# Optimization experiments

Measured on AMD Instinct MI355X. Metric: run time of the kernel, lower is better.

The kernel has to match this reference:

```python
import jax, jax.numpy as jnp
import numpy as np
import math

RES = 320
DECIMATION = 4
M = RES * RES // DECIMATION  # 25600 trajectory points
OVERSAMP = 1.25
WIDTH = 4
BETA = math.pi * (((WIDTH / OVERSAMP) * (OVERSAMP - 0.5)) ** 2 - 0.8) ** 0.5
B = 16


def setup_inputs() -> dict:
    key = jax.random.key(0)
    k1, k2 = jax.random.split(key)
    k_space_input = jax.random.normal(k1, (B, 1, RES, RES, 2), dtype=jnp.float32)
    # learnable k-space trajectory, coords in [-RES/2, RES/2)
    trajectory = (jax.random.uniform(k2, (M, 2), dtype=jnp.float32) - 0.5) * RES
    return {"k_space_input": k_space_input, "trajectory": trajectory}


def _grid_sample_bilinear(img, traj):
    # img: [B, C, H, W]; traj: [M, 2] = (x, y) in [-res/2, res/2]
    # Matches torch grid_sample(align_corners=True, padding_mode='zeros')
    # after normalizing traj by (res/2).
    Bn, C, H, W = img.shape
    gx = traj[:, 0] / (W / 2)
    gy = traj[:, 1] / (H / 2)
    px = (gx + 1.0) * 0.5 * (W - 1)
    py = (gy + 1.0) * 0.5 * (H - 1)
    x0 = jnp.floor(px)
    y0 = jnp.floor(py)
    wx1 = px - x0
    wy1 = py - y0
    out = jnp.zeros((Bn, C, traj.shape[0]), img.dtype)
    for dy in (0, 1):
        for dx in (0, 1):
            xi = x0 + dx
            yi = y0 + dy
            w = (wx1 if dx else 1.0 - wx1) * (wy1 if dy else 1.0 - wy1)
            inb = (xi >= 0) & (xi < W) & (yi >= 0) & (yi < H)
            xc = jnp.clip(xi, 0, W - 1).astype(jnp.int32)
            yc = jnp.clip(yi, 0, H - 1).astype(jnp.int32)
            out = out + img[:, :, yc, xc] * (w * inb)[None, None, :]
    return out  # [B, C, M]


def _kb_weight(delta, half):
    # Kaiser-Bessel interpolation kernel (sigpy convention, 1/width factor per dim)
    x = delta / half
    t = jnp.maximum(1.0 - x * x, 0.0)
    return jnp.i0(BETA * jnp.sqrt(t)) / WIDTH


def _nufft_adjoint(y, coord, H, W):
    # y: [B, M] complex64; coord: [M,2], coord[:,0]->H axis, coord[:,1]->W axis
    osH = math.ceil(OVERSAMP * H)
    osW = math.ceil(OVERSAMP * W)
    scale = jnp.array([osH / H, osW / W], jnp.float32)
    shift = jnp.array([osH // 2, osW // 2], jnp.float32)
    c = coord * scale + shift  # scaled to oversampled-grid coords
    half = WIDTH / 2.0
    start = jnp.ceil(c - half)                       # [M,2]
    offs = jnp.arange(WIDTH, dtype=jnp.float32)
    idx = start[:, :, None] + offs                   # [M,2,WIDTH]
    w = _kb_weight(c[:, :, None] - idx, half)        # [M,2,WIDTH]
    iy = idx[:, 0].astype(jnp.int32) % osH           # [M,WIDTH]
    ix = idx[:, 1].astype(jnp.int32) % osW
    ww = w[:, 0, :, None] * w[:, 1, None, :]         # [M,WIDTH,WIDTH]
    flat = (iy[:, :, None] * osW + ix[:, None, :]).reshape(-1)  # [M*WIDTH^2]
    Bn = y.shape[0]
    contrib = (y[:, :, None, None] * ww[None]).reshape(Bn, -1)  # [B, M*WIDTH^2]
    grid = jnp.zeros((Bn, osH * osW), y.dtype).at[:, flat].add(contrib)
    grid = grid.reshape(Bn, osH, osW)
    # centered unnormalized-to-ortho IFFT (sigpy scaling)
    img = jnp.fft.fftshift(
        jnp.fft.ifft2(jnp.fft.ifftshift(grid, axes=(-2, -1)), axes=(-2, -1)),
        axes=(-2, -1))
    img = img * ((osH * osW) / math.sqrt(H * W))
    sy = osH // 2 - H // 2
    sx = osW // 2 - W // 2
    img = img[:, sy:sy + H, sx:sx + W]  # center crop

    def apod(n, os_n):
        a = jnp.sqrt(jnp.maximum(
            BETA ** 2 - (np.pi * WIDTH * (jnp.arange(n, dtype=jnp.float32) - n // 2) / os_n) ** 2,
            1e-12))
        return a / jnp.sinh(a)

    img = img * apod(H, osH)[:, None] * apod(W, osW)[None, :]
    return img  # [B, H, W] complex


def reference(k_space_input, trajectory):
    # [B,1,H,W,2] -> [B,2,H,W] (real/imag channels)
    ksp = jnp.transpose(k_space_input, (0, 1, 4, 2, 3))[:, 0]
    sub = _grid_sample_bilinear(ksp, trajectory)          # [B,2,M]
    y = (sub[:, 0] + 1j * sub[:, 1]).astype(jnp.complex64)
    img = _nufft_adjoint(y, trajectory, ksp.shape[-2], ksp.shape[-1])
    out = jnp.stack([img.real, img.imag], axis=1)          # [B,2,H,W]
    return out[:, None]                                    # [B,1,2,H,W]
```

## Files before the change

### kernel.cpp

```cpp
#include <hip/hip_runtime.h>

#define NPTS   25600
#define NB     16
#define NRES   320
#define OS     400
#define NCELL  (OS * OS)
#define CAP    16
#define MAXOVF 4096

#define NJ     8
#define FFTTH  512
#define LSTRV  404

#define BETA_F (3.14159265358979f * 2.22710574513201f)

__device__ __forceinline__ float bessel_i0f(float x) {
    float ax = fabsf(x);
    if (ax < 3.75f) {
        float t = (ax * ax) * (1.0f / 14.0625f);
        return 1.0f + t * (3.5156229f + t * (3.0899424f + t * (1.2067492f +
                     t * (0.2659732f + t * (0.0360768f + t * 0.0045813f)))));
    } else {
        float t = 3.75f / ax;
        return (expf(ax) * rsqrtf(ax)) *
               (0.39894228f + t * (0.01328592f + t * (0.00225319f + t * (-0.00157565f +
                t * (0.00916281f + t * (-0.02057706f + t * (0.02635537f +
                t * (-0.01647633f + t * 0.00392377f))))))));
    }
}

struct OvfEntry { int cell; int m; float w; float pad; };

__global__ __launch_bounds__(256)
void k_sample(const float* __restrict__ ksp,
              const float* __restrict__ traj,
              float2* __restrict__ val)
{
    int gid = blockIdx.x * blockDim.x + threadIdx.x;
    if (gid >= NPTS * NB) return;
    int b = gid & 15;
    int m = gid >> 4;

    float tx = traj[2 * m + 0];
    float ty = traj[2 * m + 1];

    float px = (tx * (1.0f / 160.0f) + 1.0f) * 0.5f * 319.0f;
    float py = (ty * (1.0f / 160.0f) + 1.0f) * 0.5f * 319.0f;
    float fx0 = floorf(px), fy0 = floorf(py);
    int x0 = (int)fx0, y0 = (int)fy0;
    float wx1 = px - fx0, wy1 = py - fy0;
    float wx0 = 1.0f - wx1, wy0 = 1.0f - wy1;
    x0 = min(max(x0, 0), NRES - 1);
    y0 = min(max(y0, 0), NRES - 1);
    int x1 = min(x0 + 1, NRES - 1);
    int y1 = min(y0 + 1, NRES - 1);

    const float2* base = (const float2*)ksp + (size_t)b * NRES * NRES;
    float2 v00 = base[y0 * NRES + x0];
    float2 v01 = base[y0 * NRES + x1];
    float2 v10 = base[y1 * NRES + x0];
    float2 v11 = base[y1 * NRES + x1];
    float sr = (v00.x * wx0 + v01.x * wx1) * wy0 + (v10.x * wx0 + v11.x * wx1) * wy1;
    float si = (v00.y * wx0 + v01.y * wx1) * wy0 + (v10.y * wx0 + v11.y * wx1) * wy1;

    val[gid] = make_float2(sr, si);
}

__global__ __launch_bounds__(256)
void k_taps(const float* __restrict__ traj,
            int* __restrict__ cursor,
            float2* __restrict__ entries,
            int* __restrict__ ovf_cnt,
            OvfEntry* __restrict__ ovf)
{
    int m = blockIdx.x * blockDim.x + threadIdx.x;
    if (m >= NPTS) return;

    float tx = traj[2 * m + 0];
    float ty = traj[2 * m + 1];
    float c0 = tx * 1.25f + 200.0f;
    float c1 = ty * 1.25f + 200.0f;
    float s0 = ceilf(c0 - 2.0f);
    float s1 = ceilf(c1 - 2.0f);

    float w0[4], w1[4];
    int   i0[4], i1[4];
#pragma unroll
    for (int t = 0; t < 4; t++) {
        float id0 = s0 + (float)t;
        float d0 = (c0 - id0) * 0.5f;
        float t0 = fmaxf(1.0f - d0 * d0, 0.0f);
        w0[t] = bessel_i0f(BETA_F * sqrtf(t0)) * 0.25f;
        i0[t] = (((int)id0) + OS) % OS;

        float id1 = s1 + (float)t;
        float d1 = (c1 - id1) * 0.5f;
        float t1 = fmaxf(1.0f - d1 * d1, 0.0f);
        w1[t] = bessel_i0f(BETA_F * sqrtf(t1)) * 0.25f;
        i1[t] = (((int)id1) + OS) % OS;
    }

#pragma unroll
    for (int t0 = 0; t0 < 4; t0++) {
#pragma unroll
        for (int t1 = 0; t1 < 4; t1++) {
            int cell = i1[t1] * OS + i0[t0];
            float w = w0[t0] * w1[t1];
            int slot = atomicAdd(&cursor[cell], 1);
            if (slot < CAP) {
                entries[slot * NCELL + cell] = make_float2(__int_as_float(m), w);
            } else {
                int oi = atomicAdd(ovf_cnt, 1);
                if (oi < MAXOVF) { ovf[oi].cell = cell; ovf[oi].m = m; ovf[oi].w = w; }
            }
        }
    }
}

__global__ __launch_bounds__(256)
void k_gather(const int* __restrict__ cursor,
              const float2* __restrict__ entries,
              const float4* __restrict__ val4,
              float2* __restrict__ grid,
              const int* __restrict__ ovf_cnt,
              const OvfEntry* __restrict__ ovf)
{
    int cell = blockIdx.x * blockDim.x + threadIdx.x;
    if (cell >= NCELL) return;
    int cnt_raw = cursor[cell];
    int cnt = min(cnt_raw, CAP);

    float4 acc[8];
#pragma unroll
    for (int q = 0; q < 8; q++) acc[q] = make_float4(0.f, 0.f, 0.f, 0.f);

    for (int k = 0; k < cnt; k++) {
        float2 e = entries[k * NCELL + cell];
        int m = __float_as_int(e.x);
        float w = e.y;
        const float4* v = val4 + (size_t)m * 8;
#pragma unroll
        for (int q = 0; q < 8; q++) {
            float4 x = v[q];
            acc[q].x = fmaf(w, x.x, acc[q].x);
            acc[q].y = fmaf(w, x.y, acc[q].y);
            acc[q].z = fmaf(w, x.z, acc[q].z);
            acc[q].w = fmaf(w, x.w, acc[q].w);
        }
    }

    if (cnt_raw > CAP) {
        int n = min(*ovf_cnt, MAXOVF);
        for (int i = 0; i < n; i++) {
            if (ovf[i].cell != cell) continue;
            int m = ovf[i].m;
            float w = ovf[i].w;
            const float4* v = val4 + (size_t)m * 8;
#pragma unroll
            for (int q = 0; q < 8; q++) {
                float4 x = v[q];
                acc[q].x = fmaf(w, x.x, acc[q].x);
                acc[q].y = fmaf(w, x.y, acc[q].y);
                acc[q].z = fmaf(w, x.z, acc[q].z);
                acc[q].w = fmaf(w, x.w, acc[q].w);
            }
        }
    }

#pragma unroll
    for (int q = 0; q < 8; q++) {
        grid[(size_t)(2 * q + 0) * NCELL + cell] = make_float2(acc[q].x, acc[q].y);
        grid[(size_t)(2 * q + 1) * NCELL + cell] = make_float2(acc[q].z, acc[q].w);
    }
}


__device__ __forceinline__ float apodf(int i) {
    float t = (float)(i - 160) * 0.031415926535897932f;
    float a = sqrtf(fmaxf(BETA_F * BETA_F - t * t, 1e-12f));
    return a / sinhf(a);
}

__global__ __launch_bounds__(FFTTH)
void k_fft_pass_a(const float* __restrict__ grid, float* __restrict__ At)
{
    __shared__ float2 A[NJ * LSTRV];
    __shared__ float4 B4[NJ * 200];
    __shared__ float2 E20t[20];
    __shared__ float2 E400p[424];
    int tid = threadIdx.x;
    int b = blockIdx.y;
    int j0 = blockIdx.x * NJ;

    for (int t = tid; t < 400; t += FFTTH) {
        float sn, cs;
        sincosf((float)t * 0.015707963267948966f, &sn, &cs);
        E400p[t + (t >> 4)] = make_float2(cs, sn);
    }
    if (tid < 20) {
        float sn, cs;
        sincosf((float)tid * 0.3141592653589793f, &sn, &cs);
        E20t[tid] = make_float2(cs, sn);
    }
    const float2* g = (const float2*)grid + ((size_t)b * OS + j0) * OS;
    for (int o = tid; o < NJ * OS; o += FFTTH) {
        int r = o / OS, i = o - r * OS;
        A[r * LSTRV + i] = g[r * OS + i];
    }
    __syncthreads();

    for (int o = tid; o < NJ * 200; o += FFTTH) {
        int r = o / 200, rem = o - r * 200;
        int j = rem / 20, n2 = rem - j * 20;
        const float2* Al = &A[r * LSTRV];
        float4 outv;
        if (j == 0) {
            float2 a0 = Al[n2], a1 = Al[n2 + 200];
            outv = make_float4(a0.x, a0.y, a1.x, a1.y);
        } else {
            float2 a0 = Al[n2 + 20 * j], a1 = Al[n2 + 20 * (20 - j)];
            outv = make_float4(a0.x + a1.x, a0.y + a1.y, a0.x - a1.x, a0.y - a1.y);
        }
        B4[r * 200 + j * 20 + n2] = outv;
    }
    __syncthreads();

    for (int o = tid; o < NJ * 200; o += FFTTH) {
        int r = o / 200, rem = o - r * 200;
        int k1h = rem / 20, n2 = rem - k1h * 20;
        const float4* Bl = &B4[r * 200];
        float4 b0 = Bl[n2];
        float2* Ar_ = &A[r * LSTRV + 20 * n2];
        if (k1h == 0) {
            float b_r = b0.x + b0.z, b_i = b0.y + b0.w;
            float a0r = 0.f, a0i = 0.f, d0r = 0.f, d0i = 0.f;
#pragma unroll
            for (int j = 1; j <= 9; j++) {
                float4 P = Bl[j * 20 + n2];
                a0r += P.x; a0i += P.y;
                float sg = (j & 1) ? -1.f : 1.f;
                d0r = fmaf(sg, P.x, d0r); d0i = fmaf(sg, P.y, d0i);
            }
            Ar_[0] = make_float2(b_r + a0r, b_i + a0i);
            int ti = 10 * n2;
            float2 tw = E400p[ti + (ti >> 4)];
            float xr = b_r + d0r, xi = b_i + d0i;
            Ar_[10] = make_float2(xr * tw.x - xi * tw.y, xr * tw.y + xi * tw.x);
        } else {
            float sgn = (k1h & 1) ? -1.f : 1.f;
            float b_r = fmaf(sgn, b0.z, b0.x), b_i = fmaf(sgn, b0.w, b0.y);
            float2 ek = E20t[k1h];
            float c = ek.x, s = ek.y;
            float Asr = 0.f, Asi = 0.f, Bsr = 0.f, Bsi = 0.f;
#pragma unroll
            for (int j = 1; j <= 9; j++) {
                float4 P = Bl[j * 20 + n2];
                Asr = fmaf(c, P.x, Asr); Asi = fmaf(c, P.y, Asi);
                Bsr = fmaf(s, P.w, Bsr); Bsi = fmaf(s, P.z, Bsi);
                float cn = c * ek.x - s * ek.y;
                s = c * ek.y + s * ek.x;
                c = cn;
            }
            float x1r = b_r + Asr - Bsr, x1i = b_i + Asi + Bsi;
            float x2r = b_r + Asr + Bsr, x2i = b_i + Asi - Bsi;
            int t1 = n2 * k1h;
            int t2 = n2 * (20 - k1h);
            float2 tw1 = E400p[t1 + (t1 >> 4)];
            float2 tw2 = E400p[t2 + (t2 >> 4)];
            Ar_[k1h]      = make_float2(x1r * tw1.x - x1i * tw1.y, x1r * tw1.y + x1i * tw1.x);
            Ar_[20 - k1h] = make_float2(x2r * tw2.x - x2i * tw2.y, x2r * tw2.y + x2i * tw2.x);
        }
    }
    __syncthreads();

    for (int o = tid; o < NJ * 200; o += FFTTH) {
        int r = o / 200, rem = o - r * 200;
        int j = rem / 20, k1 = rem - j * 20;
        const float2* Sl = &A[r * LSTRV];
        float4 outv;
        if (j == 0) {
            float2 a0 = Sl[k1], a1 = Sl[200 + k1];
            outv = make_float4(a0.x, a0.y, a1.x, a1.y);
        } else {
            float2 a0 = Sl[20 * j + k1], a1 = Sl[20 * (20 - j) + k1];
            outv = make_float4(a0.x + a1.x, a0.y + a1.y, a0.x - a1.x, a0.y - a1.y);
        }
        B4[r * 200 + j * 20 + k1] = outv;
    }
    __syncthreads();

    for (int o = tid; o < NJ * 180; o += FFTTH) {
        int r = o / 180, rem = o - r * 180;
        int k2h = rem / 20, k1 = rem - k2h * 20;
        const float4* Bl = &B4[r * 200];
        float4 b0 = Bl[k1];
        float2* Ar_ = &A[r * LSTRV];
        if (k2h == 0) {
            float b_r = b0.x + b0.z, b_i = b0.y + b0.w;
            float a0r = 0.f, a0i = 0.f;
#pragma unroll
            for (int j = 1; j <= 9; j++) {
                float4 P = Bl[j * 20 + k1];
                a0r += P.x; a0i += P.y;
            }
            Ar_[k1] = make_float2(b_r + a0r, b_i + a0i);
        } else {
            float sgn = (k2h & 1) ? -1.f : 1.f;
            float b_r = fmaf(sgn, b0.z, b0.x), b_i = fmaf(sgn, b0.w, b0.y);
            float2 ek = E20t[k2h];
            float c = ek.x, s = ek.y;
            float Asr = 0.f, Asi = 0.f, Bsr = 0.f, Bsi = 0.f;
#pragma unroll
            for (int j = 1; j <= 9; j++) {
                float4 P = Bl[j * 20 + k1];
                Asr = fmaf(c, P.x, Asr); Asi = fmaf(c, P.y, Asi);
                Bsr = fmaf(s, P.w, Bsr); Bsi = fmaf(s, P.z, Bsi);
                float cn = c * ek.x - s * ek.y;
                s = c * ek.y + s * ek.x;
                c = cn;
            }
            if (k2h <= 7)
                Ar_[20 * k2h + k1] = make_float2(b_r + Asr - Bsr, b_i + Asi + Bsi);
            Ar_[320 - 20 * k2h + k1] = make_float2(b_r + Asr + Bsr, b_i + Asi - Bsi);
        }
    }
    __syncthreads();

    float2* At2 = (float2*)At;
    for (int o = tid; o < 320 * NJ; o += FFTTH) {
        int uc = o >> 3, r = o & 7;
        At2[((size_t)b * 320 + uc) * OS + j0 + r] = A[r * LSTRV + uc];
    }
}

__global__ __launch_bounds__(FFTTH)
void k_fft_pass_b(const float* __restrict__ At, float* __restrict__ out)
{
    __shared__ float2 A[NJ * LSTRV];
    __shared__ float4 B4[NJ * 200];
    __shared__ float2 E20t[20];
    __shared__ float2 E400p[424];
    __shared__ float apodT[320];
    int tid = threadIdx.x;
    int b = blockIdx.y;
    int uc0 = blockIdx.x * NJ;

    for (int t = tid; t < 400; t += FFTTH) {
        float sn, cs;
        sincosf((float)t * 0.015707963267948966f, &sn, &cs);
        E400p[t + (t >> 4)] = make_float2(cs, sn);
    }
    if (tid < 20) {
        float sn, cs;
        sincosf((float)tid * 0.3141592653589793f, &sn, &cs);
        E20t[tid] = make_float2(cs, sn);
    }
    for (int t = tid; t < 320; t += FFTTH) apodT[t] = apodf(t);

    const float2* a = (const float2*)At + ((size_t)b * 320 + uc0) * OS;
    for (int o = tid; o < NJ * OS; o += FFTTH) {
        int r = o / OS, j = o - r * OS;
        A[r * LSTRV + j] = a[r * OS + j];
    }
    __syncthreads();

    for (int o = tid; o < NJ * 200; o += FFTTH) {
        int r = o / 200, rem = o - r * 200;
        int j = rem / 20, n2 = rem - j * 20;
        const float2* Al = &A[r * LSTRV];
        float4 outv;
        if (j == 0) {
            float2 a0 = Al[n2], a1 = Al[n2 + 200];
            outv = make_float4(a0.x, a0.y, a1.x, a1.y);
        } else {
            float2 a0 = Al[n2 + 20 * j], a1 = Al[n2 + 20 * (20 - j)];
            outv = make_float4(a0.x + a1.x, a0.y + a1.y, a0.x - a1.x, a0.y - a1.y);
        }
        B4[r * 200 + j * 20 + n2] = outv;
    }
    __syncthreads();

    for (int o = tid; o < NJ * 200; o += FFTTH) {
        int r = o / 200, rem = o - r * 200;
        int k1h = rem / 20, n2 = rem - k1h * 20;
        const float4* Bl = &B4[r * 200];
        float4 b0 = Bl[n2];
        float2* Ar_ = &A[r * LSTRV + 20 * n2];
        if (k1h == 0) {
            float b_r = b0.x + b0.z, b_i = b0.y + b0.w;
            float a0r = 0.f, a0i = 0.f, d0r = 0.f, d0i = 0.f;
#pragma unroll
            for (int j = 1; j <= 9; j++) {
                float4 P = Bl[j * 20 + n2];
                a0r += P.x; a0i += P.y;
                float sg = (j & 1) ? -1.f : 1.f;
                d0r = fmaf(sg, P.x, d0r); d0i = fmaf(sg, P.y, d0i);
            }
            Ar_[0] = make_float2(b_r + a0r, b_i + a0i);
            int ti = 10 * n2;
            float2 tw = E400p[ti + (ti >> 4)];
            float xr = b_r + d0r, xi = b_i + d0i;
            Ar_[10] = make_float2(xr * tw.x - xi * tw.y, xr * tw.y + xi * tw.x);
        } else {
            float sgn = (k1h & 1) ? -1.f : 1.f;
            float b_r = fmaf(sgn, b0.z, b0.x), b_i = fmaf(sgn, b0.w, b0.y);
            float2 ek = E20t[k1h];
            float c = ek.x, s = ek.y;
            float Asr = 0.f, Asi = 0.f, Bsr = 0.f, Bsi = 0.f;
#pragma unroll
            for (int j = 1; j <= 9; j++) {
                float4 P = Bl[j * 20 + n2];
                Asr = fmaf(c, P.x, Asr); Asi = fmaf(c, P.y, Asi);
                Bsr = fmaf(s, P.w, Bsr); Bsi = fmaf(s, P.z, Bsi);
                float cn = c * ek.x - s * ek.y;
                s = c * ek.y + s * ek.x;
                c = cn;
            }
            float x1r = b_r + Asr - Bsr, x1i = b_i + Asi + Bsi;
            float x2r = b_r + Asr + Bsr, x2i = b_i + Asi - Bsi;
            int t1 = n2 * k1h;
            int t2 = n2 * (20 - k1h);
            float2 tw1 = E400p[t1 + (t1 >> 4)];
            float2 tw2 = E400p[t2 + (t2 >> 4)];
            Ar_[k1h]      = make_float2(x1r * tw1.x - x1i * tw1.y, x1r * tw1.y + x1i * tw1.x);
            Ar_[20 - k1h] = make_float2(x2r * tw2.x - x2i * tw2.y, x2r * tw2.y + x2i * tw2.x);
        }
    }
    __syncthreads();

    for (int o = tid; o < NJ * 200; o += FFTTH) {
        int r = o / 200, rem = o - r * 200;
        int j = rem / 20, k1 = rem - j * 20;
        const float2* Sl = &A[r * LSTRV];
        float4 outv;
        if (j == 0) {
            float2 a0 = Sl[k1], a1 = Sl[200 + k1];
            outv = make_float4(a0.x, a0.y, a1.x, a1.y);
        } else {
            float2 a0 = Sl[20 * j + k1], a1 = Sl[20 * (20 - j) + k1];
            outv = make_float4(a0.x + a1.x, a0.y + a1.y, a0.x - a1.x, a0.y - a1.y);
        }
        B4[r * 200 + j * 20 + k1] = outv;
    }
    __syncthreads();

    for (int o = tid; o < NJ * 180; o += FFTTH) {
        int r = o / 180, rem = o - r * 180;
        int k2h = rem / 20, k1 = rem - k2h * 20;
        const float4* Bl = &B4[r * 200];
        float4 b0 = Bl[k1];
        int y = uc0 + r + 160; if (y >= 320) y -= 320;
        float apy = (1.0f / 320.0f) * apodT[y];
        float* o0 = out + (((size_t)b * 2 + 0) * NRES + y) * NRES;
        float* o1 = out + (((size_t)b * 2 + 1) * NRES + y) * NRES;
        if (k2h == 0) {
            float b_r = b0.x + b0.z, b_i = b0.y + b0.w;
            float a0r = 0.f, a0i = 0.f;
#pragma unroll
            for (int j = 1; j <= 9; j++) {
                float4 P = Bl[j * 20 + k1];
                a0r += P.x; a0i += P.y;
            }
            int vc = k1;
            int x = vc + 160; if (x >= 320) x -= 320;
            float sg = ((x + y) & 1) ? -1.0f : 1.0f;
            float sc = sg * apy * apodT[x];
            o0[x] = (b_r + a0r) * sc;
            o1[x] = (b_i + a0i) * sc;
        } else {
            float sgn = (k2h & 1) ? -1.f : 1.f;
            float b_r = fmaf(sgn, b0.z, b0.x), b_i = fmaf(sgn, b0.w, b0.y);
            float2 ek = E20t[k2h];
            float c = ek.x, s = ek.y;
            float Asr = 0.f, Asi = 0.f, Bsr = 0.f, Bsi = 0.f;
#pragma unroll
            for (int j = 1; j <= 9; j++) {
                float4 P = Bl[j * 20 + k1];
                Asr = fmaf(c, P.x, Asr); Asi = fmaf(c, P.y, Asi);
                Bsr = fmaf(s, P.w, Bsr); Bsi = fmaf(s, P.z, Bsi);
                float cn = c * ek.x - s * ek.y;
                s = c * ek.y + s * ek.x;
                c = cn;
            }
            if (k2h <= 7) {
                int vc = 20 * k2h + k1;
                int x = vc + 160; if (x >= 320) x -= 320;
                float sg = ((x + y) & 1) ? -1.0f : 1.0f;
                float sc = sg * apy * apodT[x];
                o0[x] = (b_r + Asr - Bsr) * sc;
                o1[x] = (b_i + Asi + Bsi) * sc;
            }
            {
                int vc = 320 - 20 * k2h + k1;
                int x = vc + 160; if (x >= 320) x -= 320;
                float sg = ((x + y) & 1) ? -1.0f : 1.0f;
                float sc = sg * apy * apodT[x];
                o0[x] = (b_r + Asr + Bsr) * sc;
                o1[x] = (b_i + Asi - Bsi) * sc;
            }
        }
    }
}

extern "C" void kernel_launch(void* const* d_in, const int* in_sizes, int n_in,
                              void* d_out, int out_size, void* d_ws, size_t ws_size,
                              hipStream_t stream) {
    const float* ksp  = (const float*)d_in[0];
    const float* traj = (const float*)d_in[1];
    float* out = (float*)d_out;

    float* grid = (float*)d_ws;
    float* At   = grid + (size_t)NB * NCELL * 2;
    float2* entries = (float2*)At;
    float2* val = (float2*)(At + (size_t)NB * NCELL * 2);
    int* cursor  = (int*)(val + (size_t)NPTS * NB);
    int* ovf_cnt = cursor + NCELL;
    OvfEntry* ovf = (OvfEntry*)(ovf_cnt + 16);

    hipMemsetAsync(cursor, 0, (NCELL + 16) * sizeof(int), stream);

    k_sample    <<<dim3((NPTS * NB) / 256), 256, 0, stream>>>(ksp, traj, val);
    k_taps      <<<dim3(NPTS / 256), 256, 0, stream>>>(traj, cursor, entries, ovf_cnt, ovf);
    k_gather    <<<dim3((NCELL + 255) / 256), 256, 0, stream>>>(cursor, entries, (const float4*)val,
                                                                (float2*)grid, ovf_cnt, ovf);
    k_fft_pass_a<<<dim3(OS / NJ, NB),  FFTTH, 0, stream>>>(grid, At);
    k_fft_pass_b<<<dim3(320 / NJ, NB), FFTTH, 0, stream>>>(At, out);
}
```

Before: 155.9 us.

## Merge sample and tap kernels; fuse gridding gather into first FFT pass

Combines the bilinear sampling and Kaiser-Bessel tap-binning kernels into one launch split by block index. Removes the separate gather kernel and the intermediate oversampled grid buffer by having the first FFT pass gather each cell's contributions directly into shared memory. This saves two launches and a full grid write and read. In exchange, each FFT block re-reads the cursor and entry lists once per batch (16 times in total instead of once), using scalar float2 value loads.

```diff
diff --git a/kernel.cpp b/kernel.cpp
--- a/kernel.cpp
+++ b/kernel.cpp
@@ -32,145 +32,86 @@
 struct OvfEntry { int cell; int m; float w; float pad; };
 
 __global__ __launch_bounds__(256)
-void k_sample(const float* __restrict__ ksp,
-              const float* __restrict__ traj,
-              float2* __restrict__ val)
+void k_sample_taps(const float* __restrict__ ksp,
+                   const float* __restrict__ traj,
+                   float2* __restrict__ val,
+                   int* __restrict__ cursor,
+                   float2* __restrict__ entries,
+                   int* __restrict__ ovf_cnt,
+                   OvfEntry* __restrict__ ovf)
 {
-    int gid = blockIdx.x * blockDim.x + threadIdx.x;
-    if (gid >= NPTS * NB) return;
-    int b = gid & 15;
-    int m = gid >> 4;
-
-    float tx = traj[2 * m + 0];
-    float ty = traj[2 * m + 1];
-
-    float px = (tx * (1.0f / 160.0f) + 1.0f) * 0.5f * 319.0f;
-    float py = (ty * (1.0f / 160.0f) + 1.0f) * 0.5f * 319.0f;
-    float fx0 = floorf(px), fy0 = floorf(py);
-    int x0 = (int)fx0, y0 = (int)fy0;
-    float wx1 = px - fx0, wy1 = py - fy0;
-    float wx0 = 1.0f - wx1, wy0 = 1.0f - wy1;
-    x0 = min(max(x0, 0), NRES - 1);
-    y0 = min(max(y0, 0), NRES - 1);
-    int x1 = min(x0 + 1, NRES - 1);
-    int y1 = min(y0 + 1, NRES - 1);
-
-    const float2* base = (const float2*)ksp + (size_t)b * NRES * NRES;
-    float2 v00 = base[y0 * NRES + x0];
-    float2 v01 = base[y0 * NRES + x1];
-    float2 v10 = base[y1 * NRES + x0];
-    float2 v11 = base[y1 * NRES + x1];
-    float sr = (v00.x * wx0 + v01.x * wx1) * wy0 + (v10.x * wx0 + v11.x * wx1) * wy1;
-    float si = (v00.y * wx0 + v01.y * wx1) * wy0 + (v10.y * wx0 + v11.y * wx1) * wy1;
-
-    val[gid] = make_float2(sr, si);
-}
-
-__global__ __launch_bounds__(256)
-void k_taps(const float* __restrict__ traj,
-            int* __restrict__ cursor,
-            float2* __restrict__ entries,
-            int* __restrict__ ovf_cnt,
-            OvfEntry* __restrict__ ovf)
-{
-    int m = blockIdx.x * blockDim.x + threadIdx.x;
-    if (m >= NPTS) return;
-
-    float tx = traj[2 * m + 0];
-    float ty = traj[2 * m + 1];
-    float c0 = tx * 1.25f + 200.0f;
-    float c1 = ty * 1.25f + 200.0f;
-    float s0 = ceilf(c0 - 2.0f);
-    float s1 = ceilf(c1 - 2.0f);
-
-    float w0[4], w1[4];
-    int   i0[4], i1[4];
-#pragma unroll
-    for (int t = 0; t < 4; t++) {
-        float id0 = s0 + (float)t;
-        float d0 = (c0 - id0) * 0.5f;
-        float t0 = fmaxf(1.0f - d0 * d0, 0.0f);
-        w0[t] = bessel_i0f(BETA_F * sqrtf(t0)) * 0.25f;
-        i0[t] = (((int)id0) + OS) % OS;
-
-        float id1 = s1 + (float)t;
-        float d1 = (c1 - id1) * 0.5f;
-        float t1 = fmaxf(1.0f - d1 * d1, 0.0f);
-        w1[t] = bessel_i0f(BETA_F * sqrtf(t1)) * 0.25f;
-        i1[t] = (((int)id1) + OS) % OS;
-    }
-
-#pragma unroll
-    for (int t0 = 0; t0 < 4; t0++) {
-#pragma unroll
-        for (int t1 = 0; t1 < 4; t1++) {
-            int cell = i1[t1] * OS + i0[t0];
-            float w = w0[t0] * w1[t1];
-            int slot = atomicAdd(&cursor[cell], 1);
-            if (slot < CAP) {
-                entries[slot * NCELL + cell] = make_float2(__int_as_float(m), w);
-            } else {
-                int oi = atomicAdd(ovf_cnt, 1);
-                if (oi < MAXOVF) { ovf[oi].cell = cell; ovf[oi].m = m; ovf[oi].w = w; }
-            }
-        }
-    }
-}
-
-__global__ __launch_bounds__(256)
-void k_gather(const int* __restrict__ cursor,
-              const float2* __restrict__ entries,
-              const float4* __restrict__ val4,
-              float2* __restrict__ grid,
-              const int* __restrict__ ovf_cnt,
-              const OvfEntry* __restrict__ ovf)
-{
-    int cell = blockIdx.x * blockDim.x + threadIdx.x;
-    if (cell >= NCELL) return;
-    int cnt_raw = cursor[cell];
-    int cnt = min(cnt_raw, CAP);
-
-    float4 acc[8];
-#pragma unroll
-    for (int q = 0; q < 8; q++) acc[q] = make_float4(0.f, 0.f, 0.f, 0.f);
-
-    for (int k = 0; k < cnt; k++) {
-        float2 e = entries[k * NCELL + cell];
-        int m = __float_as_int(e.x);
-        float w = e.y;
-        const float4* v = val4 + (size_t)m * 8;
-#pragma unroll
-        for (int q = 0; q < 8; q++) {
-            float4 x = v[q];
-            acc[q].x = fmaf(w, x.x, acc[q].x);
-            acc[q].y = fmaf(w, x.y, acc[q].y);
-            acc[q].z = fmaf(w, x.z, acc[q].z);
-            acc[q].w = fmaf(w, x.w, acc[q].w);
-        }
-    }
-
-    if (cnt_raw > CAP) {
-        int n = min(*ovf_cnt, MAXOVF);
-        for (int i = 0; i < n; i++) {
-            if (ovf[i].cell != cell) continue;
-            int m = ovf[i].m;
-            float w = ovf[i].w;
-            const float4* v = val4 + (size_t)m * 8;
-#pragma unroll
-            for (int q = 0; q < 8; q++) {
-                float4 x = v[q];
-                acc[q].x = fmaf(w, x.x, acc[q].x);
-                acc[q].y = fmaf(w, x.y, acc[q].y);
-                acc[q].z = fmaf(w, x.z, acc[q].z);
-                acc[q].w = fmaf(w, x.w, acc[q].w);
-            }
-        }
-    }
-
-#pragma unroll
-    for (int q = 0; q < 8; q++) {
-        grid[(size_t)(2 * q + 0) * NCELL + cell] = make_float2(acc[q].x, acc[q].y);
-        grid[(size_t)(2 * q + 1) * NCELL + cell] = make_float2(acc[q].z, acc[q].w);
+    int blk = blockIdx.x;
+    if (blk < 1600) {
+        int gid = blk * 256 + threadIdx.x;
+        int b = gid & 15;
+        int m = gid >> 4;
+
+        float tx = traj[2 * m + 0];
+        float ty = traj[2 * m + 1];
+
+        float px = (tx * (1.0f / 160.0f) + 1.0f) * 0.5f * 319.0f;
+        float py = (ty * (1.0f / 160.0f) + 1.0f) * 0.5f * 319.0f;
+        float fx0 = floorf(px), fy0 = floorf(py);
+        int x0 = (int)fx0, y0 = (int)fy0;
+        float wx1 = px - fx0, wy1 = py - fy0;
+        float wx0 = 1.0f - wx1, wy0 = 1.0f - wy1;
+        x0 = min(max(x0, 0), NRES - 1);
+        y0 = min(max(y0, 0), NRES - 1);
+        int x1 = min(x0 + 1, NRES - 1);
+        int y1 = min(y0 + 1, NRES - 1);
+
+        const float2* base = (const float2*)ksp + (size_t)b * NRES * NRES;
+        float2 v00 = base[y0 * NRES + x0];
+        float2 v01 = base[y0 * NRES + x1];
+        float2 v10 = base[y1 * NRES + x0];
+        float2 v11 = base[y1 * NRES + x1];
+        float sr = (v00.x * wx0 + v01.x * wx1) * wy0 + (v10.x * wx0 + v11.x * wx1) * wy1;
+        float si = (v00.y * wx0 + v01.y * wx1) * wy0 + (v10.y * wx0 + v11.y * wx1) * wy1;
+
+        val[gid] = make_float2(sr, si);
+    } else {
+        int m = (blk - 1600) * 256 + threadIdx.x;
+        if (m >= NPTS) return;
+
+        float tx = traj[2 * m + 0];
+        float ty = traj[2 * m + 1];
+        float c0 = tx * 1.25f + 200.0f;
+        float c1 = ty * 1.25f + 200.0f;
+        float s0 = ceilf(c0 - 2.0f);
+        float s1 = ceilf(c1 - 2.0f);
+
+        float w0[4], w1[4];
+        int   i0[4], i1[4];
+#pragma unroll
+        for (int t = 0; t < 4; t++) {
+            float id0 = s0 + (float)t;
+            float d0 = (c0 - id0) * 0.5f;
+            float t0 = fmaxf(1.0f - d0 * d0, 0.0f);
+            w0[t] = bessel_i0f(BETA_F * sqrtf(t0)) * 0.25f;
+            i0[t] = (((int)id0) + OS) % OS;
+
+            float id1 = s1 + (float)t;
+            float d1 = (c1 - id1) * 0.5f;
+            float t1 = fmaxf(1.0f - d1 * d1, 0.0f);
+            w1[t] = bessel_i0f(BETA_F * sqrtf(t1)) * 0.25f;
+            i1[t] = (((int)id1) + OS) % OS;
+        }
+
+#pragma unroll
+        for (int t0 = 0; t0 < 4; t0++) {
+#pragma unroll
+            for (int t1 = 0; t1 < 4; t1++) {
+                int cell = i1[t1] * OS + i0[t0];
+                float w = w0[t0] * w1[t1];
+                int slot = atomicAdd(&cursor[cell], 1);
+                if (slot < CAP) {
+                    entries[(size_t)slot * NCELL + cell] = make_float2(__int_as_float(m), w);
+                } else {
+                    int oi = atomicAdd(ovf_cnt, 1);
+                    if (oi < MAXOVF) { ovf[oi].cell = cell; ovf[oi].m = m; ovf[oi].w = w; }
+                }
+            }
+        }
     }
 }
 
@@ -182,7 +123,12 @@
 }
 
 __global__ __launch_bounds__(FFTTH)
-void k_fft_pass_a(const float* __restrict__ grid, float* __restrict__ At)
+void k_fft_pass_a(const int* __restrict__ cursor,
+                  const float2* __restrict__ entries,
+                  const float2* __restrict__ val,
+                  const int* __restrict__ ovf_cnt,
+                  const OvfEntry* __restrict__ ovf,
+                  float* __restrict__ At)
 {
     __shared__ float2 A[NJ * LSTRV];
     __shared__ float4 B4[NJ * 200];
@@ -202,10 +148,32 @@
         sincosf((float)tid * 0.3141592653589793f, &sn, &cs);
         E20t[tid] = make_float2(cs, sn);
     }
-    const float2* g = (const float2*)grid + ((size_t)b * OS + j0) * OS;
+
     for (int o = tid; o < NJ * OS; o += FFTTH) {
         int r = o / OS, i = o - r * OS;
-        A[r * LSTRV + i] = g[r * OS + i];
+        int cell = (j0 + r) * OS + i;
+        int cnt_raw = cursor[cell];
+        int cnt = min(cnt_raw, CAP);
+        float ar = 0.f, ai = 0.f;
+        for (int k = 0; k < cnt; k++) {
+            float2 e = entries[(size_t)k * NCELL + cell];
+            int m = __float_as_int(e.x);
+            float w = e.y;
+            float2 x = val[(size_t)m * NB + b];
+            ar = fmaf(w, x.x, ar);
+            ai = fmaf(w, x.y, ai);
+        }
+        if (cnt_raw > CAP) {
+            int n = min(*ovf_cnt, MAXOVF);
+            for (int q = 0; q < n; q++) {
+                if (ovf[q].cell == cell) {
+                    float2 x = val[(size_t)ovf[q].m * NB + b];
+                    ar = fmaf(ovf[q].w, x.x, ar);
+                    ai = fmaf(ovf[q].w, x.y, ai);
+                }
+            }
+        }
+        A[r * LSTRV + i] = make_float2(ar, ai);
     }
     __syncthreads();
 
@@ -461,8 +429,7 @@
                 float4 P = Bl[j * 20 + k1];
                 a0r += P.x; a0i += P.y;
             }
-            int vc = k1;
-            int x = vc + 160; if (x >= 320) x -= 320;
+            int x = k1 + 160; if (x >= 320) x -= 320;
             float sg = ((x + y) & 1) ? -1.0f : 1.0f;
             float sc = sg * apy * apodT[x];
             o0[x] = (b_r + a0r) * sc;
@@ -509,20 +476,16 @@
     const float* traj = (const float*)d_in[1];
     float* out = (float*)d_out;
 
-    float* grid = (float*)d_ws;
-    float* At   = grid + (size_t)NB * NCELL * 2;
-    float2* entries = (float2*)At;
-    float2* val = (float2*)(At + (size_t)NB * NCELL * 2);
+    float* At = (float*)d_ws;
+    float2* entries = (float2*)(At + (size_t)NB * 320 * OS * 2);
+    float2* val = (float2*)(entries + (size_t)CAP * NCELL);
     int* cursor  = (int*)(val + (size_t)NPTS * NB);
     int* ovf_cnt = cursor + NCELL;
     OvfEntry* ovf = (OvfEntry*)(ovf_cnt + 16);
 
     hipMemsetAsync(cursor, 0, (NCELL + 16) * sizeof(int), stream);
 
-    k_sample    <<<dim3((NPTS * NB) / 256), 256, 0, stream>>>(ksp, traj, val);
-    k_taps      <<<dim3(NPTS / 256), 256, 0, stream>>>(traj, cursor, entries, ovf_cnt, ovf);
-    k_gather    <<<dim3((NCELL + 255) / 256), 256, 0, stream>>>(cursor, entries, (const float4*)val,
-                                                                (float2*)grid, ovf_cnt, ovf);
-    k_fft_pass_a<<<dim3(OS / NJ, NB),  FFTTH, 0, stream>>>(grid, At);
-    k_fft_pass_b<<<dim3(320 / NJ, NB), FFTTH, 0, stream>>>(At, out);
-}
+    k_sample_taps<<<dim3(1700), 256, 0, stream>>>(ksp, traj, val, cursor, entries, ovf_cnt, ovf);
+    k_fft_pass_a <<<dim3(OS / NJ, NB),  FFTTH, 0, stream>>>(cursor, entries, val, ovf_cnt, ovf, At);
+    k_fft_pass_b <<<dim3(320 / NJ, NB), FFTTH, 0, stream>>>(At, out);
+}
```

Measured after the change: 186.6 us. +19.7%, slower.

## Fuse sample and tap-binning kernels into one launch and vectorize FFT row loads

Applied to the files above, without the earlier changes.

Merges the bilinear sampling kernel and the Kaiser-Bessel tap-binning kernel into one launch, where block ranges are split between the two independent jobs. This saves one kernel launch and lets the two jobs overlap on the device. The FFT passes now load rows into LDS as float4 instead of float2, halving the number of load instructions. The workspace is rearranged so the entries buffer no longer aliases At, and index arithmetic is widened to size_t.

```diff
diff --git a/kernel.cpp b/kernel.cpp
--- a/kernel.cpp
+++ b/kernel.cpp
@@ -32,86 +32,84 @@
 struct OvfEntry { int cell; int m; float w; float pad; };
 
 __global__ __launch_bounds__(256)
-void k_sample(const float* __restrict__ ksp,
-              const float* __restrict__ traj,
-              float2* __restrict__ val)
+void k_sample_taps(const float* __restrict__ ksp,
+                   const float* __restrict__ traj,
+                   float2* __restrict__ val,
+                   int* __restrict__ cursor,
+                   float2* __restrict__ entries,
+                   int* __restrict__ ovf_cnt,
+                   OvfEntry* __restrict__ ovf)
 {
-    int gid = blockIdx.x * blockDim.x + threadIdx.x;
-    if (gid >= NPTS * NB) return;
-    int b = gid & 15;
-    int m = gid >> 4;
-
-    float tx = traj[2 * m + 0];
-    float ty = traj[2 * m + 1];
-
-    float px = (tx * (1.0f / 160.0f) + 1.0f) * 0.5f * 319.0f;
-    float py = (ty * (1.0f / 160.0f) + 1.0f) * 0.5f * 319.0f;
-    float fx0 = floorf(px), fy0 = floorf(py);
-    int x0 = (int)fx0, y0 = (int)fy0;
-    float wx1 = px - fx0, wy1 = py - fy0;
-    float wx0 = 1.0f - wx1, wy0 = 1.0f - wy1;
-    x0 = min(max(x0, 0), NRES - 1);
-    y0 = min(max(y0, 0), NRES - 1);
-    int x1 = min(x0 + 1, NRES - 1);
-    int y1 = min(y0 + 1, NRES - 1);
-
-    const float2* base = (const float2*)ksp + (size_t)b * NRES * NRES;
-    float2 v00 = base[y0 * NRES + x0];
-    float2 v01 = base[y0 * NRES + x1];
-    float2 v10 = base[y1 * NRES + x0];
-    float2 v11 = base[y1 * NRES + x1];
-    float sr = (v00.x * wx0 + v01.x * wx1) * wy0 + (v10.x * wx0 + v11.x * wx1) * wy1;
-    float si = (v00.y * wx0 + v01.y * wx1) * wy0 + (v10.y * wx0 + v11.y * wx1) * wy1;
-
-    val[gid] = make_float2(sr, si);
-}
-
-__global__ __launch_bounds__(256)
-void k_taps(const float* __restrict__ traj,
-            int* __restrict__ cursor,
-            float2* __restrict__ entries,
-            int* __restrict__ ovf_cnt,
-            OvfEntry* __restrict__ ovf)
-{
-    int m = blockIdx.x * blockDim.x + threadIdx.x;
-    if (m >= NPTS) return;
-
-    float tx = traj[2 * m + 0];
-    float ty = traj[2 * m + 1];
-    float c0 = tx * 1.25f + 200.0f;
-    float c1 = ty * 1.25f + 200.0f;
-    float s0 = ceilf(c0 - 2.0f);
-    float s1 = ceilf(c1 - 2.0f);
-
-    float w0[4], w1[4];
-    int   i0[4], i1[4];
-#pragma unroll
-    for (int t = 0; t < 4; t++) {
-        float id0 = s0 + (float)t;
-        float d0 = (c0 - id0) * 0.5f;
-        float t0 = fmaxf(1.0f - d0 * d0, 0.0f);
-        w0[t] = bessel_i0f(BETA_F * sqrtf(t0)) * 0.25f;
-        i0[t] = (((int)id0) + OS) % OS;
-
-        float id1 = s1 + (float)t;
-        float d1 = (c1 - id1) * 0.5f;
-        float t1 = fmaxf(1.0f - d1 * d1, 0.0f);
-        w1[t] = bessel_i0f(BETA_F * sqrtf(t1)) * 0.25f;
-        i1[t] = (((int)id1) + OS) % OS;
-    }
-
-#pragma unroll
-    for (int t0 = 0; t0 < 4; t0++) {
-#pragma unroll
-        for (int t1 = 0; t1 < 4; t1++) {
-            int cell = i1[t1] * OS + i0[t0];
-            float w = w0[t0] * w1[t1];
-            int slot = atomicAdd(&cursor[cell], 1);
-            if (slot < CAP) {
-                entries[slot * NCELL + cell] = make_float2(__int_as_float(m), w);
-            } else {
-                int oi = atomicAdd(ovf_cnt, 1);
-                if (oi < MAXOVF) { ovf[oi].cell = cell; ovf[oi].m = m; ovf[oi].w = w; }
+    int blk = blockIdx.x;
+    if (blk < 1600) {
+        int gid = blk * 256 + threadIdx.x;
+        int b = gid & 15;
+        int m = gid >> 4;
+
+        float tx = traj[2 * m + 0];
+        float ty = traj[2 * m + 1];
+
+        float px = (tx * (1.0f / 160.0f) + 1.0f) * 0.5f * 319.0f;
+        float py = (ty * (1.0f / 160.0f) + 1.0f) * 0.5f * 319.0f;
+        float fx0 = floorf(px), fy0 = floorf(py);
+        int x0 = (int)fx0, y0 = (int)fy0;
+        float wx1 = px - fx0, wy1 = py - fy0;
+        float wx0 = 1.0f - wx1, wy0 = 1.0f - wy1;
+        x0 = min(max(x0, 0), NRES - 1);
+        y0 = min(max(y0, 0), NRES - 1);
+        int x1 = min(x0 + 1, NRES - 1);
+        int y1 = min(y0 + 1, NRES - 1);
+
+        const float2* base = (const float2*)ksp + (size_t)b * NRES * NRES;
+        float2 v00 = base[y0 * NRES + x0];
+        float2 v01 = base[y0 * NRES + x1];
+        float2 v10 = base[y1 * NRES + x0];
+        float2 v11 = base[y1 * NRES + x1];
+        float sr = (v00.x * wx0 + v01.x * wx1) * wy0 + (v10.x * wx0 + v11.x * wx1) * wy1;
+        float si = (v00.y * wx0 + v01.y * wx1) * wy0 + (v10.y * wx0 + v11.y * wx1) * wy1;
+
+        val[gid] = make_float2(sr, si);
+    } else {
+        int m = (blk - 1600) * 256 + threadIdx.x;
+        if (m >= NPTS) return;
+
+        float tx = traj[2 * m + 0];
+        float ty = traj[2 * m + 1];
+        float c0 = tx * 1.25f + 200.0f;
+        float c1 = ty * 1.25f + 200.0f;
+        float s0 = ceilf(c0 - 2.0f);
+        float s1 = ceilf(c1 - 2.0f);
+
+        float w0[4], w1[4];
+        int   i0[4], i1[4];
+#pragma unroll
+        for (int t = 0; t < 4; t++) {
+            float id0 = s0 + (float)t;
+            float d0 = (c0 - id0) * 0.5f;
+            float t0 = fmaxf(1.0f - d0 * d0, 0.0f);
+            w0[t] = bessel_i0f(BETA_F * sqrtf(t0)) * 0.25f;
+            i0[t] = (((int)id0) + OS) % OS;
+
+            float id1 = s1 + (float)t;
+            float d1 = (c1 - id1) * 0.5f;
+            float t1 = fmaxf(1.0f - d1 * d1, 0.0f);
+            w1[t] = bessel_i0f(BETA_F * sqrtf(t1)) * 0.25f;
+            i1[t] = (((int)id1) + OS) % OS;
+        }
+
+#pragma unroll
+        for (int t0 = 0; t0 < 4; t0++) {
+#pragma unroll
+            for (int t1 = 0; t1 < 4; t1++) {
+                int cell = i1[t1] * OS + i0[t0];
+                float w = w0[t0] * w1[t1];
+                int slot = atomicAdd(&cursor[cell], 1);
+                if (slot < CAP) {
+                    entries[(size_t)slot * NCELL + cell] = make_float2(__int_as_float(m), w);
+                } else {
+                    int oi = atomicAdd(ovf_cnt, 1);
+                    if (oi < MAXOVF) { ovf[oi].cell = cell; ovf[oi].m = m; ovf[oi].w = w; }
+                }
             }
         }
     }
@@ -135,7 +133,7 @@
     for (int q = 0; q < 8; q++) acc[q] = make_float4(0.f, 0.f, 0.f, 0.f);
 
     for (int k = 0; k < cnt; k++) {
-        float2 e = entries[k * NCELL + cell];
+        float2 e = entries[(size_t)k * NCELL + cell];
         int m = __float_as_int(e.x);
         float w = e.y;
         const float4* v = val4 + (size_t)m * 8;
@@ -202,10 +200,10 @@
         sincosf((float)tid * 0.3141592653589793f, &sn, &cs);
         E20t[tid] = make_float2(cs, sn);
     }
-    const float2* g = (const float2*)grid + ((size_t)b * OS + j0) * OS;
-    for (int o = tid; o < NJ * OS; o += FFTTH) {
-        int r = o / OS, i = o - r * OS;
-        A[r * LSTRV + i] = g[r * OS + i];
+    const float4* g4 = (const float4*)(grid + ((size_t)b * NCELL + (size_t)j0 * OS) * 2);
+    for (int o = tid; o < NJ * 200; o += FFTTH) {
+        int r = o / 200, q = o - r * 200;
+        *((float4*)&A[r * LSTRV] + q) = g4[r * 200 + q];
     }
     __syncthreads();
 
@@ -357,10 +355,10 @@
     }
     for (int t = tid; t < 320; t += FFTTH) apodT[t] = apodf(t);
 
-    const float2* a = (const float2*)At + ((size_t)b * 320 + uc0) * OS;
-    for (int o = tid; o < NJ * OS; o += FFTTH) {
-        int r = o / OS, j = o - r * OS;
-        A[r * LSTRV + j] = a[r * OS + j];
+    const float4* a4 = (const float4*)(At + ((size_t)b * 320 + uc0) * OS * 2);
+    for (int o = tid; o < NJ * 200; o += FFTTH) {
+        int r = o / 200, q = o - r * 200;
+        *((float4*)&A[r * LSTRV] + q) = a4[r * 200 + q];
     }
     __syncthreads();
 
@@ -461,8 +459,7 @@
                 float4 P = Bl[j * 20 + k1];
                 a0r += P.x; a0i += P.y;
             }
-            int vc = k1;
-            int x = vc + 160; if (x >= 320) x -= 320;
+            int x = k1 + 160; if (x >= 320) x -= 320;
             float sg = ((x + y) & 1) ? -1.0f : 1.0f;
             float sc = sg * apy * apodT[x];
             o0[x] = (b_r + a0r) * sc;
@@ -511,18 +508,17 @@
 
     float* grid = (float*)d_ws;
     float* At   = grid + (size_t)NB * NCELL * 2;
-    float2* entries = (float2*)At;
-    float2* val = (float2*)(At + (size_t)NB * NCELL * 2);
+    float2* entries = (float2*)(At + (size_t)NB * 320 * OS * 2);
+    float2* val = (float2*)(entries + (size_t)CAP * NCELL);
     int* cursor  = (int*)(val + (size_t)NPTS * NB);
     int* ovf_cnt = cursor + NCELL;
     OvfEntry* ovf = (OvfEntry*)(ovf_cnt + 16);
 
     hipMemsetAsync(cursor, 0, (NCELL + 16) * sizeof(int), stream);
 
-    k_sample    <<<dim3((NPTS * NB) / 256), 256, 0, stream>>>(ksp, traj, val);
-    k_taps      <<<dim3(NPTS / 256), 256, 0, stream>>>(traj, cursor, entries, ovf_cnt, ovf);
-    k_gather    <<<dim3((NCELL + 255) / 256), 256, 0, stream>>>(cursor, entries, (const float4*)val,
-                                                                (float2*)grid, ovf_cnt, ovf);
-    k_fft_pass_a<<<dim3(OS / NJ, NB),  FFTTH, 0, stream>>>(grid, At);
-    k_fft_pass_b<<<dim3(320 / NJ, NB), FFTTH, 0, stream>>>(At, out);
-}
+    k_sample_taps<<<dim3(1700), 256, 0, stream>>>(ksp, traj, val, cursor, entries, ovf_cnt, ovf);
+    k_gather     <<<dim3((NCELL + 255) / 256), 256, 0, stream>>>(cursor, entries, (const float4*)val,
+                                                                 (float2*)grid, ovf_cnt, ovf);
+    k_fft_pass_a <<<dim3(OS / NJ, NB),  FFTTH, 0, stream>>>(grid, At);
+    k_fft_pass_b <<<dim3(320 / NJ, NB), FFTTH, 0, stream>>>(At, out);
+}
```

Result: faster. 149.6 us (-4.0%).
